# Kernel tuning notes

Measured on AMD Instinct MI355X. Metric: run time of the kernel, lower is better.

## Reference

```python
import jax, jax.numpy as jnp
import numpy as np

B, L, D, OUT, EXP = 4, 4096, 128, 55, 2
D2 = 2 * D

def _ln(x, g, b):
    m = jnp.mean(x, axis=-1, keepdims=True)
    v = jnp.mean((x - m) ** 2, axis=-1, keepdims=True)
    return (x - m) / jnp.sqrt(v + 1e-5) * g + b

def setup_inputs() -> dict:
    key = jax.random.key(0)
    ks = iter(jax.random.split(key, 32))
    w = lambda shape: jax.random.normal(next(ks), shape, jnp.float32) * 0.02
    inp = {
        'x1': jax.random.normal(next(ks), (B, L, D), jnp.float32),
        'x2': jax.random.normal(next(ks), (B, L, D), jnp.float32),
        'ln1_g': jnp.ones((D,)), 'ln1_b': jnp.zeros((D,)),
        'ln2_g': jnp.ones((D,)), 'ln2_b': jnp.zeros((D,)),
        'Wq': w((D, D)), 'bq': jnp.zeros((D,)),
        'Wv1': w((D, D)), 'bv1': jnp.zeros((D,)),
        'Wk': w((D, D)), 'bk': jnp.zeros((D,)),
        'Wv2': w((D, D)), 'bv2': jnp.zeros((D,)),
        'Wp1': w((D, D)), 'bp1': jnp.zeros((D,)),
        'Wp2': w((D, D)), 'bp2': jnp.zeros((D,)),
        'lnf_g': jnp.ones((D2,)), 'lnf_b': jnp.zeros((D2,)),
        'Wf1': w((D2, EXP * D2)), 'bf1': jnp.zeros((EXP * D2,)),
        'Wf2': w((EXP * D2, D2)), 'bf2': jnp.zeros((D2,)),
        'ln3_g': jnp.ones((D2,)), 'ln3_b': jnp.zeros((D2,)),
        'Wo': w((D2, OUT)), 'bo': jnp.zeros((OUT,)),
    }
    return inp

def reference(x1, x2, ln1_g, ln1_b, ln2_g, ln2_b, Wq, bq, Wv1, bv1, Wk, bk,
              Wv2, bv2, Wp1, bp1, Wp2, bp2, lnf_g, lnf_b, Wf1, bf1, Wf2, bf2,
              ln3_g, ln3_b, Wo, bo):
    res1, res2 = x1, x2
    x1n = _ln(x1, ln1_g, ln1_b)
    x2n = _ln(x2, ln2_g, ln2_b)
    q1 = x1n @ Wq + bq        # [B,L,D]
    v1 = x1n @ Wv1 + bv1
    k2 = x2n @ Wk + bk
    v2 = x2n @ Wv2 + bv2
    # faithful to torch: energy = einsum('bqd,bkd->bqk', keys2, queries1)
    energy = jnp.einsum('bqd,bkd->bqk', k2, q1)
    att = jax.nn.softmax(energy / jnp.sqrt(jnp.float32(D)), axis=-1)  # [B,L,L]
    out1 = jnp.einsum('bal,blv->bav', att, v1) @ Wp1 + bp1
    out2 = jnp.einsum('bal,blv->bav', att, v2) @ Wp2 + bp2
    y1 = out1 + res1
    y2 = out2 + res2
    x = jnp.concatenate([y1, y2], axis=-1)  # [B,L,2D]
    res = x
    h = _ln(x, lnf_g, lnf_b)
    h = jax.nn.gelu(h @ Wf1 + bf1, approximate=False) @ Wf2 + bf2
    x = _ln(h + res, ln3_g, ln3_b)
    return x @ Wo + bo  # [B,L,OUT]
```

## Files before the change

kernel.cpp:

```cpp
#include <hip/hip_runtime.h>
#include <hip/hip_fp16.h>

typedef _Float16 half8 __attribute__((ext_vector_type(8)));
typedef _Float16 half4 __attribute__((ext_vector_type(4)));
typedef float f32x4 __attribute__((ext_vector_type(4)));
typedef float f32x16 __attribute__((ext_vector_type(16)));
typedef int  i32x8 __attribute__((ext_vector_type(8)));
typedef long lng2 __attribute__((ext_vector_type(2)));

#define B_   4
#define L_   4096
#define D_   128
#define M_   (B_*L_)
#define D2_  256
#define H_   512
#define OUT_ 55

__device__ __forceinline__ f32x4 mfma16(half8 a, half8 b, f32x4 c) {
    return __builtin_amdgcn_mfma_f32_16x16x32_f16(a, b, c, 0, 0, 0);
}
__device__ __forceinline__ f32x16 mfma_mx32(i32x8 a, i32x8 b, f32x16 c) {
    return __builtin_amdgcn_mfma_scale_f32_32x32x64_f8f6f4(a, b, c, 0, 0, 0, 127, 0, 127);
}
__device__ __forceinline__ int pk4(float a, float b, float c, float d) {
    int t = __builtin_amdgcn_cvt_pk_fp8_f32(a, b, 0, false);
    return __builtin_amdgcn_cvt_pk_fp8_f32(c, d, t, true);
}
__device__ __forceinline__ float fexp2(float x) { return __builtin_amdgcn_exp2f(x); }

#define KSCL (0.08838834764831845f * 1.4426950408889634f)

#define WQ_OFF   0
#define WV1_OFF  16384
#define WK_OFF   32768
#define WV2_OFF  49152
#define WP1_OFF  65536
#define WP2_OFF  81920
#define WF1_OFF  98304
#define WF2_OFF  229376
#define WO_OFF   360448


__global__ void prep_kernel(const float* Wq, const float* Wv1, const float* Wk,
                            const float* Wv2, const float* Wp1, const float* Wp2,
                            const float* Wf1, const float* Wf2, const float* Wo,
                            _Float16* wsw, float* rowsum) {
    int id = blockIdx.y;
    int t  = blockIdx.x * 256 + threadIdx.x;
    if (id == 9) {
        if (t < 4096) ((f32x4*)rowsum)[t] = f32x4{0.f, 0.f, 0.f, 0.f};
        return;
    }
    const float* src = nullptr; int K = 0, N = 0, Npad = 0, off = 0;
    switch (id) {
        case 0: src = Wq;  K = 128; N = 128; Npad = 128; off = WQ_OFF;  break;
        case 1: src = Wv1; K = 128; N = 128; Npad = 128; off = WV1_OFF; break;
        case 2: src = Wk;  K = 128; N = 128; Npad = 128; off = WK_OFF;  break;
        case 3: src = Wv2; K = 128; N = 128; Npad = 128; off = WV2_OFF; break;
        case 4: src = Wp1; K = 128; N = 128; Npad = 128; off = WP1_OFF; break;
        case 5: src = Wp2; K = 128; N = 128; Npad = 128; off = WP2_OFF; break;
        case 6: src = Wf1; K = 256; N = 512; Npad = 512; off = WF1_OFF; break;
        case 7: src = Wf2; K = 512; N = 256; Npad = 256; off = WF2_OFF; break;
        case 8: src = Wo;  K = 256; N = 55;  Npad = 64;  off = WO_OFF;  break;
        default: return;
    }
    int total = K * Npad;
    if (t >= total) return;
    int k = t / Npad, n = t % Npad;
    float v = (n < N) ? src[k * N + n] : 0.f;
    int s = k >> 5, c = n >> 4, ln = n & 15;
    int q, j;
    if (id == 4 || id == 5) { q = (k >> 2) & 3; j = (k & 3) + (((k >> 4) & 1) << 2); }
    else                    { q = (k >> 3) & 3; j = k & 7; }
    int nc = Npad >> 4;
    wsw[off + ((size_t)((s * nc + c) * 64 + q * 16 + ln)) * 8 + j] = (_Float16)v;
}


__global__ __launch_bounds__(256) void proj_kernel(const float* x1, const float* x2,
        const _Float16* wsw,
        const float* ln1_g, const float* ln1_b, const float* ln2_g, const float* ln2_b,
        const float* bq, const float* bv1, const float* bk, const float* bv2,
        _Float16* q1, _Float16* k2, unsigned char* vsw8) {
    int g2 = blockIdx.y;
    const float* X  = g2 ? x2 : x1;
    const float* lg = g2 ? ln2_g : ln1_g;
    const float* lb = g2 ? ln2_b : ln1_b;
    int wave = threadIdx.x >> 6, lane = threadIdx.x & 63;
    int quad = lane >> 4, ln = lane & 15;
    int mbase = blockIdx.x * 64 + wave * 16;
    int lt = mbase >> 4;

    const float* xr = X + (size_t)(mbase + ln) * D_;
    float xv[4][8];
    float sum = 0.f, sq = 0.f;
    #pragma unroll
    for (int s = 0; s < 4; s++) {
        f32x4 v0 = *(const f32x4*)(xr + s * 32 + quad * 8);
        f32x4 v1 = *(const f32x4*)(xr + s * 32 + quad * 8 + 4);
        #pragma unroll
        for (int j = 0; j < 4; j++) {
            xv[s][j]     = v0[j];
            xv[s][j + 4] = v1[j];
            sum += v0[j] + v1[j];
            sq  += v0[j] * v0[j] + v1[j] * v1[j];
        }
    }
    sum += __shfl_xor(sum, 16); sum += __shfl_xor(sum, 32);
    sq  += __shfl_xor(sq, 16);  sq  += __shfl_xor(sq, 32);
    float mean = sum * (1.f / 128.f);
    float var  = sq * (1.f / 128.f) - mean * mean;
    float inv  = rsqrtf(var + 1e-5f);
    half8 a[4];
    #pragma unroll
    for (int s = 0; s < 4; s++) {
        f32x4 g0 = *(const f32x4*)(lg + s * 32 + quad * 8);
        f32x4 g1 = *(const f32x4*)(lg + s * 32 + quad * 8 + 4);
        f32x4 b0 = *(const f32x4*)(lb + s * 32 + quad * 8);
        f32x4 b1 = *(const f32x4*)(lb + s * 32 + quad * 8 + 4);
        #pragma unroll
        for (int j = 0; j < 4; j++) {
            a[s][j]     = (_Float16)((xv[s][j] - mean) * inv * g0[j] + b0[j]);
            a[s][j + 4] = (_Float16)((xv[s][j + 4] - mean) * inv * g1[j] + b1[j]);
        }
    }

    {
        const _Float16* Bw = wsw + (g2 ? WK_OFF : WQ_OFF);
        const float* bias = g2 ? bk : bq;
        float scl = g2 ? KSCL : 1.f;
        _Float16* out = g2 ? k2 : q1;
        f32x4 acc[8];
        #pragma unroll
        for (int c = 0; c < 8; c++) acc[c] = f32x4{0.f, 0.f, 0.f, 0.f};
        half8 Wc[4], Wn[4];
        #pragma unroll
        for (int s = 0; s < 4; s++)
            Wc[s] = *(const half8*)(Bw + ((size_t)((s * 8 + 0) * 64 + lane)) * 8);
        #pragma unroll
        for (int c = 0; c < 8; c++) {
            int cn = (c < 7) ? c + 1 : 7;
            #pragma unroll
            for (int s = 0; s < 4; s++)
                Wn[s] = *(const half8*)(Bw + ((size_t)((s * 8 + cn) * 64 + lane)) * 8);
            #pragma unroll
            for (int s = 0; s < 4; s++)
                acc[c] = mfma16(a[s], Wc[s], acc[c]);
            #pragma unroll
            for (int s = 0; s < 4; s++) Wc[s] = Wn[s];
        }
        #pragma unroll
        for (int c = 0; c < 8; c++) {
            int n = c * 16 + ln;
            float bv = bias[n];
            #pragma unroll
            for (int r = 0; r < 4; r++) {
                int s_o = c >> 1, q_o = ((c & 1) << 1) | (ln >> 3), j = ln & 7;
                out[((size_t)((lt * 4 + s_o) * 64 + q_o * 16 + (quad * 4 + r))) * 8 + j]
                    = (_Float16)((acc[c][r] + bv) * scl);
            }
        }
    }

    {
        const _Float16* Bw = wsw + (g2 ? WV2_OFF : WV1_OFF);
        const float* bias = g2 ? bv2 : bv1;
        int cbase = g2 ? 8 : 0;
        f32x4 acc[8];
        #pragma unroll
        for (int c = 0; c < 8; c++) acc[c] = f32x4{0.f, 0.f, 0.f, 0.f};
        half8 Wc[4], Wn[4];
        #pragma unroll
        for (int s = 0; s < 4; s++)
            Wc[s] = *(const half8*)(Bw + ((size_t)((s * 8 + 0) * 64 + lane)) * 8);
        #pragma unroll
        for (int c = 0; c < 8; c++) {
            int cn = (c < 7) ? c + 1 : 7;
            #pragma unroll
            for (int s = 0; s < 4; s++)
                Wn[s] = *(const half8*)(Bw + ((size_t)((s * 8 + cn) * 64 + lane)) * 8);
            #pragma unroll
            for (int s = 0; s < 4; s++)
                acc[c] = mfma16(a[s], Wc[s], acc[c]);
            #pragma unroll
            for (int s = 0; s < 4; s++) Wc[s] = Wn[s];
        }
        int b = mbase >> 12;
        int k64 = (mbase & (L_ - 1)) >> 6;
        int gg = quad >> 1, jh = quad & 1;
        unsigned char* Vb = vsw8 + (size_t)b * (1u << 20);
        #pragma unroll
        for (int c = 0; c < 8; c++) {
            int n = c * 16 + ln;
            float bv = bias[n];
            int pk = pk4(acc[c][0] + bv, acc[c][1] + bv, acc[c][2] + bv, acc[c][3] + bv);
            int v32 = (cbase + c) >> 1;
            int lane32 = ((c & 1) << 4) + ln + 32 * gg;
            *(int*)(Vb + ((size_t)((k64 * 8 + v32) * 64 + lane32)) * 32 + 16 * jh + 4 * wave) = pk;
        }
    }
}

__global__ __launch_bounds__(256) void score_kernel(
        const _Float16* __restrict__ q1sw, const _Float16* __restrict__ k2sw,
        unsigned char* __restrict__ pmat8, float* __restrict__ rowsum) {
    int w = threadIdx.x >> 6, lane = threadIdx.x & 63;
    int quad = lane >> 4, ln = lane & 15;
    int b = blockIdx.z;
    int id0 = blockIdx.y * 32 + blockIdx.x;
    int id  = ((id0 & 7) << 7) + (id0 >> 3);
    int bx = id & 31, by = id >> 5;
    int kL0 = by * 128 + (w & 1) * 64;
    int mL0 = bx * 128 + (w >> 1) * 64;
    int ltk = ((b << 12) + kL0) >> 4;
    int ltm = ((b << 12) + mL0) >> 4;

    f32x4 acc[4][4];
    #pragma unroll
    for (int i = 0; i < 4; i++)
        #pragma unroll
        for (int j = 0; j < 4; j++) acc[i][j] = f32x4{0.f, 0.f, 0.f, 0.f};

    #pragma unroll
    for (int s = 0; s < 4; s++) {
        half8 a[4], bq[4];
        #pragma unroll
        for (int i = 0; i < 4; i++)
            a[i] = *(const half8*)(q1sw + ((size_t)(((ltk + i) * 4 + s) * 64 + lane)) * 8);
        #pragma unroll
        for (int j = 0; j < 4; j++)
            bq[j] = *(const half8*)(k2sw + ((size_t)(((ltm + j) * 4 + s) * 64 + lane)) * 8);
        #pragma unroll
        for (int i = 0; i < 4; i++)
            #pragma unroll
            for (int j = 0; j < 4; j++)
                acc[i][j] = mfma16(a[i], bq[j], acc[i][j]);
    }

    unsigned char* Pb = pmat8 + (size_t)b * (16u << 20);
    int k64 = kL0 >> 6;
    int gg = quad >> 1, jh = quad & 1;
    #pragma unroll
    for (int j = 0; j < 4; j++) {
        int4 d;
        float csum = 0.f;
        #pragma unroll
        for (int i = 0; i < 4; i++) {
            float p0 = fexp2(acc[i][j][0]);
            float p1 = fexp2(acc[i][j][1]);
            float p2 = fexp2(acc[i][j][2]);
            float p3 = fexp2(acc[i][j][3]);
            csum += (p0 + p1) + (p2 + p3);
            ((int*)&d)[i] = pk4(p0, p1, p2, p3);
        }
        csum += __shfl_xor(csum, 16);
        csum += __shfl_xor(csum, 32);
        if (lane < 16)
            atomicAdd(&rowsum[(b << 12) + mL0 + j * 16 + ln], csum);
        int att32 = (mL0 >> 5) + (j >> 1);
        int a32 = ((j & 1) << 4) + ln;
        *(int4*)(Pb + ((size_t)((att32 * 64 + k64) * 64 + a32 + 32 * gg)) * 32 + 16 * jh) = d;
    }
}

__global__ __launch_bounds__(512) void pv_kernel(
        const unsigned char* __restrict__ pmat8, const unsigned char* __restrict__ vsw8,
        const float* __restrict__ rowsum,
        _Float16* __restrict__ att1, _Float16* __restrict__ att2) {
    __shared__ f32x4 part[4][2][4][64];
    int w = threadIdx.x >> 6, lane = threadIdx.x & 63;
    int wc = w & 3, kh = w >> 2;
    int id0 = blockIdx.x;
    int bid = ((id0 & 7) << 6) + (id0 >> 3);
    int rowG0 = bid * 32;
    int b = rowG0 >> 12;
    int att32 = (rowG0 & (L_ - 1)) >> 5;
    const unsigned char* Pb = pmat8 + (size_t)b * (16u << 20);
    const unsigned char* Vb = vsw8 + (size_t)b * (1u << 20);

    const unsigned char* Vbase = Vb + (size_t)(wc * 2) * 2048 + (size_t)lane * 32;
    const unsigned char* Pbase = Pb + (size_t)att32 * 131072 + (size_t)lane * 32;
    int sp0 = kh * 32;

    f32x16 acc0, acc1;
    #pragma unroll
    for (int i = 0; i < 16; i++) { acc0[i] = 0.f; acc1[i] = 0.f; }

    #define PVLOAD(dA, dB, dP, sp) do {                                       \
        dA = *(const i32x8*)(Vbase + (size_t)(sp) * 16384);                   \
        dB = *(const i32x8*)(Vbase + (size_t)(sp) * 16384 + 2048);            \
        dP = *(const i32x8*)(Pbase + (size_t)(sp) * 2048);                    \
    } while (0)

    i32x8 a0, b0, p0, a1, b1, p1, na, nb, np;
    PVLOAD(a0, b0, p0, sp0);
    PVLOAD(a1, b1, p1, sp0 + 1);
    for (int ii = 0; ii < 32; ii += 2) {
        int s2 = sp0 + ((ii + 2 < 32) ? ii + 2 : 30);
        int s3 = sp0 + ((ii + 3 < 32) ? ii + 3 : 31);
        PVLOAD(na, nb, np, s2);
        __builtin_amdgcn_s_setprio(1);
        acc0 = mfma_mx32(a0, p0, acc0);
        acc1 = mfma_mx32(b0, p0, acc1);
        __builtin_amdgcn_s_setprio(0);
        a0 = na; b0 = nb; p0 = np;
        PVLOAD(na, nb, np, s3);
        __builtin_amdgcn_s_setprio(1);
        acc0 = mfma_mx32(a1, p1, acc0);
        acc1 = mfma_mx32(b1, p1, acc1);
        __builtin_amdgcn_s_setprio(0);
        a1 = na; b1 = nb; p1 = np;
    }
    #undef PVLOAD

    if (kh == 1) {
        #pragma unroll
        for (int q = 0; q < 4; q++) {
            part[wc][0][q][lane] = f32x4{acc0[q * 4 + 0], acc0[q * 4 + 1],
                                         acc0[q * 4 + 2], acc0[q * 4 + 3]};
            part[wc][1][q][lane] = f32x4{acc1[q * 4 + 0], acc1[q * 4 + 1],
                                         acc1[q * 4 + 2], acc1[q * 4 + 3]};
        }
    }
    __syncthreads();
    if (kh == 0) {
        int aglob = rowG0 + (lane & 31);
        float inv = 1.f / rowsum[aglob];
        int g = lane >> 5;
        int lt = aglob >> 4, lnr = lane & 15;
        #pragma unroll
        for (int t = 0; t < 2; t++) {
            int v32 = wc * 2 + t;
            _Float16* att = (v32 >= 4) ? att2 : att1;
            int s = v32 & 3;
            #pragma unroll
            for (int q = 0; q < 4; q++) {
                f32x4 pp = part[wc][t][q][lane];
                half4 hv;
                #pragma unroll
                for (int rr = 0; rr < 4; rr++) {
                    float v = ((t == 0) ? acc0[q * 4 + rr] : acc1[q * 4 + rr]) + pp[rr];
                    hv[rr] = (_Float16)(v * inv);
                }
                *(half4*)(att + ((size_t)((lt * 4 + s) * 64 + q * 16 + lnr)) * 8 + 4 * g) = hv;
            }
        }
    }
}

__global__ __launch_bounds__(256) void attn_out_kernel(const _Float16* att1, const _Float16* att2,
        const _Float16* wsw, const float* bp1, const float* bp2,
        const float* x1, const float* x2, const float* lnf_g, const float* lnf_b,
        _Float16* res, _Float16* xn) {
    __shared__ float sst[2][16][2][2];
    int w = threadIdx.x >> 6, lane = threadIdx.x & 63;
    int quad = lane >> 4, ln = lane & 15;
    int rt = w & 1, st = w >> 1;
    int mbase = blockIdx.x * 32 + rt * 16;
    int lt = mbase >> 4;
    const _Float16* att = st ? att2 : att1;
    const _Float16* Wp = wsw + (st ? WP2_OFF : WP1_OFF);
    const float* bp = st ? bp2 : bp1;
    const float* xres = st ? x2 : x1;

    half8 a[4];
    #pragma unroll
    for (int s = 0; s < 4; s++)
        a[s] = *(const half8*)(att + ((size_t)((lt * 4 + s) * 64 + lane)) * 8);

    f32x4 y[8];
    #pragma unroll
    for (int c = 0; c < 8; c++) y[c] = f32x4{0,0,0,0};

    half8 Wc[4], Wn[4];
    #pragma unroll
    for (int s = 0; s < 4; s++)
        Wc[s] = *(const half8*)(Wp + ((size_t)((s * 8 + 0) * 64 + lane)) * 8);
    #pragma unroll
    for (int c = 0; c < 8; c++) {
        int cn = (c < 7) ? c + 1 : 7;
        #pragma unroll
        for (int s = 0; s < 4; s++)
            Wn[s] = *(const half8*)(Wp + ((size_t)((s * 8 + cn) * 64 + lane)) * 8);
        #pragma unroll
        for (int s = 0; s < 4; s++)
            y[c] = mfma16(a[s], Wc[s], y[c]);
        #pragma unroll
        for (int s = 0; s < 4; s++) Wc[s] = Wn[s];
    }

    float psum[4] = {0,0,0,0}, psq[4] = {0,0,0,0};
    #pragma unroll
    for (int c = 0; c < 8; c++) {
        int n = c * 16 + ln;
        float bv = bp[n];
        #pragma unroll
        for (int r = 0; r < 4; r++) {
            int m = mbase + quad * 4 + r;
            float v = y[c][r] + bv + xres[(size_t)m * D_ + n];
            y[c][r] = v; psum[r] += v; psq[r] += v * v;
        }
    }
    #pragma unroll
    for (int off = 1; off < 16; off <<= 1)
        #pragma unroll
        for (int r = 0; r < 4; r++) { psum[r] += __shfl_xor(psum[r], off); psq[r] += __shfl_xor(psq[r], off); }
    if (ln == 0)
        #pragma unroll
        for (int r = 0; r < 4; r++) {
            sst[rt][quad * 4 + r][st][0] = psum[r];
            sst[rt][quad * 4 + r][st][1] = psq[r];
        }
    __syncthreads();
    #pragma unroll
    for (int r = 0; r < 4; r++) {
        float su = sst[rt][quad * 4 + r][0][0] + sst[rt][quad * 4 + r][1][0];
        float sq = sst[rt][quad * 4 + r][0][1] + sst[rt][quad * 4 + r][1][1];
        float mean = su * (1.f / 256.f);
        float var = sq * (1.f / 256.f) - mean * mean;
        float inv = rsqrtf(var + 1e-5f);
        int m = mbase + quad * 4 + r;
        int lt_m = m >> 4;
        #pragma unroll
        for (int c = 0; c < 8; c++) {
            int colg = st * 128 + c * 16 + ln;
            res[(size_t)m * D2_ + colg] = (_Float16)y[c][r];
            float yn = (y[c][r] - mean) * inv * lnf_g[colg] + lnf_b[colg];
            int s_x = colg >> 5, q_x = (colg >> 3) & 3, j = colg & 7;
            xn[((size_t)((lt_m * 8 + s_x) * 64 + q_x * 16 + (m & 15))) * 8 + j] = (_Float16)yn;
        }
    }
}

__global__ __launch_bounds__(256) void ffn1_kernel(const _Float16* xn, const _Float16* wsw,
        const float* bf1, _Float16* h) {
    int wave = threadIdx.x >> 6, lane = threadIdx.x & 63;
    int quad = lane >> 4, ln = lane & 15;
    int mbase = blockIdx.x * 64 + wave * 16;
    int lt = mbase >> 4;
    int nt = blockIdx.y;
    const _Float16* W = wsw + WF1_OFF;

    half8 a[8];
    #pragma unroll
    for (int s = 0; s < 8; s++)
        a[s] = *(const half8*)(xn + ((size_t)((lt * 8 + s) * 64 + lane)) * 8);

    f32x4 acc[8];
    #pragma unroll
    for (int c = 0; c < 8; c++) acc[c] = f32x4{0,0,0,0};

    half8 Wc[8], Wn[8];
    #pragma unroll
    for (int s = 0; s < 8; s++)
        Wc[s] = *(const half8*)(W + ((size_t)((s * 32 + nt * 8) * 64 + lane)) * 8);
    #pragma unroll
    for (int c = 0; c < 8; c++) {
        int cn = (c < 7) ? c + 1 : 7;
        #pragma unroll
        for (int s = 0; s < 8; s++)
            Wn[s] = *(const half8*)(W + ((size_t)((s * 32 + nt * 8 + cn) * 64 + lane)) * 8);
        #pragma unroll
        for (int s = 0; s < 8; s++)
            acc[c] = mfma16(a[s], Wc[s], acc[c]);
        #pragma unroll
        for (int s = 0; s < 8; s++) Wc[s] = Wn[s];
    }
    #pragma unroll
    for (int c = 0; c < 8; c++) {
        int n = nt * 128 + c * 16 + ln;
        float bv = bf1[n];
        int s_h = n >> 5, q_h = (n >> 3) & 3, j = n & 7;
        #pragma unroll
        for (int r = 0; r < 4; r++) {
            float v = acc[c][r] + bv;
            float u = 0.7978845608f * (v + 0.044715f * v * v * v);
            float e = fexp2(-2.8853900818f * u);
            float ge = v * __builtin_amdgcn_rcpf(1.f + e);
            h[((size_t)((lt * 16 + s_h) * 64 + q_h * 16 + (quad * 4 + r))) * 8 + j] = (_Float16)ge;
        }
    }
}

__global__ __launch_bounds__(256) void ffn2_out_kernel(const _Float16* h, const _Float16* wsw,
        const float* bf2, const _Float16* res, const float* g3, const float* b3,
        const float* bo, float* out) {
    __shared__ float sst[2][16][2][2];
    __shared__ _Float16 xt[8192];
    __shared__ f32x4 pc[2][4][64];
    int w = threadIdx.x >> 6, lane = threadIdx.x & 63;
    int quad = lane >> 4, ln = lane & 15;
    int rt = w & 1, nh = w >> 1;
    int mb = blockIdx.x * 32 + rt * 16;
    int lt = mb >> 4;
    const _Float16* W = wsw + WF2_OFF;

    f32x4 acc[8];
    #pragma unroll
    for (int c = 0; c < 8; c++) acc[c] = f32x4{0,0,0,0};

    half8 aC, aN;
    half8 Wc[8], Wn[8];
    aC = *(const half8*)(h + ((size_t)((lt * 16 + 0) * 64 + lane)) * 8);
    #pragma unroll
    for (int c = 0; c < 8; c++)
        Wc[c] = *(const half8*)(W + ((size_t)((0 * 16 + nh * 8 + c) * 64 + lane)) * 8);

    #pragma unroll
    for (int s = 0; s < 16; s++) {
        int sn = (s < 15) ? s + 1 : 15;
        aN = *(const half8*)(h + ((size_t)((lt * 16 + sn) * 64 + lane)) * 8);
        #pragma unroll
        for (int c = 0; c < 8; c++)
            Wn[c] = *(const half8*)(W + ((size_t)((sn * 16 + nh * 8 + c) * 64 + lane)) * 8);
        #pragma unroll
        for (int c = 0; c < 8; c++)
            acc[c] = mfma16(aC, Wc[c], acc[c]);
        aC = aN;
        #pragma unroll
        for (int c = 0; c < 8; c++) Wc[c] = Wn[c];
    }

    float y[8][4];
    float psum[4] = {0,0,0,0}, psq[4] = {0,0,0,0};
    #pragma unroll
    for (int c = 0; c < 8; c++) {
        int n = nh * 128 + c * 16 + ln;
        float bv = bf2[n];
        #pragma unroll
        for (int r = 0; r < 4; r++) {
            int m = mb + quad * 4 + r;
            float v = acc[c][r] + bv + (float)res[(size_t)m * D2_ + n];
            y[c][r] = v; psum[r] += v; psq[r] += v * v;
        }
    }
    #pragma unroll
    for (int off = 1; off < 16; off <<= 1)
        #pragma unroll
        for (int r = 0; r < 4; r++) { psum[r] += __shfl_xor(psum[r], off); psq[r] += __shfl_xor(psq[r], off); }
    if (ln == 0)
        #pragma unroll
        for (int r = 0; r < 4; r++) { sst[rt][quad * 4 + r][nh][0] = psum[r]; sst[rt][quad * 4 + r][nh][1] = psq[r]; }
    __syncthreads();
    #pragma unroll
    for (int r = 0; r < 4; r++) {
        float su = sst[rt][quad * 4 + r][0][0] + sst[rt][quad * 4 + r][1][0];
        float sq = sst[rt][quad * 4 + r][0][1] + sst[rt][quad * 4 + r][1][1];
        float mean = su * (1.f / 256.f);
        float var = sq * (1.f / 256.f) - mean * mean;
        float invs = rsqrtf(var + 1e-5f);
        #pragma unroll
        for (int c = 0; c < 8; c++) {
            int n = nh * 128 + c * 16 + ln;
            float yn = (y[c][r] - mean) * invs * g3[n] + b3[n];
            int s_x = n >> 5, q_x = (n >> 3) & 3, j = n & 7;
            xt[((rt * 8 + s_x) * 64 + q_x * 16 + (quad * 4 + r)) * 8 + j] = (_Float16)yn;
        }
    }
    __syncthreads();

    int rt2 = w & 1, kh = w >> 1;
    const _Float16* Wo = wsw + WO_OFF;
    f32x4 oacc[4];
    #pragma unroll
    for (int c = 0; c < 4; c++) oacc[c] = f32x4{0,0,0,0};
    #pragma unroll
    for (int ss = 0; ss < 4; ss++) {
        int s = kh * 4 + ss;
        half8 a = *(const half8*)(xt + ((size_t)((rt2 * 8 + s) * 64 + lane)) * 8);
        #pragma unroll
        for (int c = 0; c < 4; c++)
            oacc[c] = mfma16(a, *(const half8*)(Wo + ((size_t)((s * 4 + c) * 64 + lane)) * 8), oacc[c]);
    }
    if (kh == 1)
        #pragma unroll
        for (int c = 0; c < 4; c++) pc[rt2][c][lane] = oacc[c];
    __syncthreads();
    if (kh == 0) {
        int mb2 = blockIdx.x * 32 + rt2 * 16;
        #pragma unroll
        for (int c = 0; c < 4; c++) {
            f32x4 p = pc[rt2][c][lane];
            int n = c * 16 + ln;
            if (n < OUT_) {
                float bv = bo[n];
                #pragma unroll
                for (int r = 0; r < 4; r++)
                    out[(size_t)(mb2 + quad * 4 + r) * OUT_ + n] = oacc[c][r] + p[r] + bv;
            }
        }
    }
}

extern "C" void kernel_launch(void* const* d_in, const int* in_sizes, int n_in,
                              void* d_out, int out_size, void* d_ws, size_t ws_size,
                              hipStream_t stream) {
    const float* x1    = (const float*)d_in[0];
    const float* x2    = (const float*)d_in[1];
    const float* ln1_g = (const float*)d_in[2];
    const float* ln1_b = (const float*)d_in[3];
    const float* ln2_g = (const float*)d_in[4];
    const float* ln2_b = (const float*)d_in[5];
    const float* Wq    = (const float*)d_in[6];
    const float* bq    = (const float*)d_in[7];
    const float* Wv1   = (const float*)d_in[8];
    const float* bv1   = (const float*)d_in[9];
    const float* Wk    = (const float*)d_in[10];
    const float* bk    = (const float*)d_in[11];
    const float* Wv2   = (const float*)d_in[12];
    const float* bv2   = (const float*)d_in[13];
    const float* Wp1   = (const float*)d_in[14];
    const float* bp1   = (const float*)d_in[15];
    const float* Wp2   = (const float*)d_in[16];
    const float* bp2   = (const float*)d_in[17];
    const float* lnf_g = (const float*)d_in[18];
    const float* lnf_b = (const float*)d_in[19];
    const float* Wf1   = (const float*)d_in[20];
    const float* bf1   = (const float*)d_in[21];
    const float* Wf2   = (const float*)d_in[22];
    const float* bf2   = (const float*)d_in[23];
    const float* ln3_g = (const float*)d_in[24];
    const float* ln3_b = (const float*)d_in[25];
    const float* Wo    = (const float*)d_in[26];
    const float* bo    = (const float*)d_in[27];
    float* out = (float*)d_out;

    char* ws = (char*)d_ws;
    const size_t MB = 1 << 20;
    _Float16* q1sw   = (_Float16*)(ws + 0 * MB);
    _Float16* k2sw   = (_Float16*)(ws + 4 * MB);
    unsigned char* vsw8 = (unsigned char*)(ws + 8 * MB);
    _Float16* att1   = (_Float16*)(ws + 12 * MB);
    _Float16* att2   = (_Float16*)(ws + 16 * MB);
    _Float16* wsw    = (_Float16*)(ws + 28 * MB);
    float*    rowsum = (float*)   (ws + 29 * MB);
    _Float16* res    = (_Float16*)(ws + 30 * MB);
    _Float16* xn     = (_Float16*)(ws + 46 * MB);
    _Float16* h      = (_Float16*)(ws + 54 * MB);
    unsigned char* pmat8 = (unsigned char*)(ws + 78 * MB);

    prep_kernel<<<dim3(512, 10), 256, 0, stream>>>(Wq, Wv1, Wk, Wv2, Wp1, Wp2, Wf1, Wf2, Wo,
                                                   wsw, rowsum);
    proj_kernel<<<dim3(M_ / 64, 2), 256, 0, stream>>>(x1, x2, wsw,
                                                      ln1_g, ln1_b, ln2_g, ln2_b,
                                                      bq, bv1, bk, bv2,
                                                      q1sw, k2sw, vsw8);
    score_kernel<<<dim3(32, 32, 4), 256, 0, stream>>>(q1sw, k2sw, pmat8, rowsum);
    pv_kernel<<<dim3(M_ / 32), 512, 0, stream>>>(pmat8, vsw8, rowsum, att1, att2);
    attn_out_kernel<<<dim3(M_ / 32), 256, 0, stream>>>(att1, att2, wsw, bp1, bp2,
                                                       x1, x2, lnf_g, lnf_b, res, xn);
    ffn1_kernel<<<dim3(M_ / 64, 4), 256, 0, stream>>>(xn, wsw, bf1, h);
    ffn2_out_kernel<<<dim3(M_ / 32), 256, 0, stream>>>(h, wsw, bf2, res, ln3_g, ln3_b, bo, out);
}
```

Baseline: 233.5 us.

## Fuse FFN1 and FFN2+output kernels, keeping hidden activations in shared memory

Merges the two FFN kernels into one 512-thread block per 32 rows. The GELU hidden activations are written to a 32KB shared-memory tile instead of a global buffer, so the 16K×512 fp16 round trip and one launch go away. The work is re-split so 8 waves share the FFN2 N-dimension and the output projection K-dimension, which needs an extra partial-sum reduction. In exchange, the explicit register double-buffering of weight loads is dropped, and the larger shared-memory footprint and block size may lower occupancy.

After: 228.4 us. 2.2% less time.

```diff
diff --git a/kernel.cpp b/kernel.cpp
--- a/kernel.cpp
+++ b/kernel.cpp
@@ -432,161 +432,139 @@
     }
 }
 
-__global__ __launch_bounds__(256) void ffn1_kernel(const _Float16* xn, const _Float16* wsw,
-        const float* bf1, _Float16* h) {
-    int wave = threadIdx.x >> 6, lane = threadIdx.x & 63;
-    int quad = lane >> 4, ln = lane & 15;
-    int mbase = blockIdx.x * 64 + wave * 16;
-    int lt = mbase >> 4;
-    int nt = blockIdx.y;
-    const _Float16* W = wsw + WF1_OFF;
-
-    half8 a[8];
-    #pragma unroll
-    for (int s = 0; s < 8; s++)
-        a[s] = *(const half8*)(xn + ((size_t)((lt * 8 + s) * 64 + lane)) * 8);
-
-    f32x4 acc[8];
-    #pragma unroll
-    for (int c = 0; c < 8; c++) acc[c] = f32x4{0,0,0,0};
-
-    half8 Wc[8], Wn[8];
-    #pragma unroll
-    for (int s = 0; s < 8; s++)
-        Wc[s] = *(const half8*)(W + ((size_t)((s * 32 + nt * 8) * 64 + lane)) * 8);
-    #pragma unroll
-    for (int c = 0; c < 8; c++) {
-        int cn = (c < 7) ? c + 1 : 7;
-        #pragma unroll
-        for (int s = 0; s < 8; s++)
-            Wn[s] = *(const half8*)(W + ((size_t)((s * 32 + nt * 8 + cn) * 64 + lane)) * 8);
-        #pragma unroll
-        for (int s = 0; s < 8; s++)
-            acc[c] = mfma16(a[s], Wc[s], acc[c]);
-        #pragma unroll
-        for (int s = 0; s < 8; s++) Wc[s] = Wn[s];
-    }
-    #pragma unroll
-    for (int c = 0; c < 8; c++) {
-        int n = nt * 128 + c * 16 + ln;
-        float bv = bf1[n];
-        int s_h = n >> 5, q_h = (n >> 3) & 3, j = n & 7;
-        #pragma unroll
-        for (int r = 0; r < 4; r++) {
-            float v = acc[c][r] + bv;
-            float u = 0.7978845608f * (v + 0.044715f * v * v * v);
-            float e = fexp2(-2.8853900818f * u);
-            float ge = v * __builtin_amdgcn_rcpf(1.f + e);
-            h[((size_t)((lt * 16 + s_h) * 64 + q_h * 16 + (quad * 4 + r))) * 8 + j] = (_Float16)ge;
-        }
-    }
-}
-
-__global__ __launch_bounds__(256) void ffn2_out_kernel(const _Float16* h, const _Float16* wsw,
-        const float* bf2, const _Float16* res, const float* g3, const float* b3,
-        const float* bo, float* out) {
-    __shared__ float sst[2][16][2][2];
+__global__ __launch_bounds__(512) void ffn_kernel(const _Float16* xn, const _Float16* wsw,
+        const float* bf1, const float* bf2, const _Float16* res,
+        const float* g3, const float* b3, const float* bo, float* out) {
+    __shared__ _Float16 hT[16384];
+    __shared__ float sst[2][16][4][2];
     __shared__ _Float16 xt[8192];
-    __shared__ f32x4 pc[2][4][64];
+    __shared__ f32x4 pc[2][3][4][64];
     int w = threadIdx.x >> 6, lane = threadIdx.x & 63;
     int quad = lane >> 4, ln = lane & 15;
     int rt = w & 1, nh = w >> 1;
-    int mb = blockIdx.x * 32 + rt * 16;
-    int lt = mb >> 4;
-    const _Float16* W = wsw + WF2_OFF;
-
-    f32x4 acc[8];
-    #pragma unroll
-    for (int c = 0; c < 8; c++) acc[c] = f32x4{0,0,0,0};
-
-    half8 aC, aN;
-    half8 Wc[8], Wn[8];
-    aC = *(const half8*)(h + ((size_t)((lt * 16 + 0) * 64 + lane)) * 8);
-    #pragma unroll
-    for (int c = 0; c < 8; c++)
-        Wc[c] = *(const half8*)(W + ((size_t)((0 * 16 + nh * 8 + c) * 64 + lane)) * 8);
-
-    #pragma unroll
-    for (int s = 0; s < 16; s++) {
-        int sn = (s < 15) ? s + 1 : 15;
-        aN = *(const half8*)(h + ((size_t)((lt * 16 + sn) * 64 + lane)) * 8);
-        #pragma unroll
-        for (int c = 0; c < 8; c++)
-            Wn[c] = *(const half8*)(W + ((size_t)((sn * 16 + nh * 8 + c) * 64 + lane)) * 8);
-        #pragma unroll
-        for (int c = 0; c < 8; c++)
-            acc[c] = mfma16(aC, Wc[c], acc[c]);
-        aC = aN;
-        #pragma unroll
-        for (int c = 0; c < 8; c++) Wc[c] = Wn[c];
-    }
-
-    float y[8][4];
-    float psum[4] = {0,0,0,0}, psq[4] = {0,0,0,0};
-    #pragma unroll
-    for (int c = 0; c < 8; c++) {
-        int n = nh * 128 + c * 16 + ln;
-        float bv = bf2[n];
-        #pragma unroll
-        for (int r = 0; r < 4; r++) {
-            int m = mb + quad * 4 + r;
-            float v = acc[c][r] + bv + (float)res[(size_t)m * D2_ + n];
-            y[c][r] = v; psum[r] += v; psq[r] += v * v;
-        }
-    }
-    #pragma unroll
-    for (int off = 1; off < 16; off <<= 1)
-        #pragma unroll
-        for (int r = 0; r < 4; r++) { psum[r] += __shfl_xor(psum[r], off); psq[r] += __shfl_xor(psq[r], off); }
-    if (ln == 0)
-        #pragma unroll
-        for (int r = 0; r < 4; r++) { sst[rt][quad * 4 + r][nh][0] = psum[r]; sst[rt][quad * 4 + r][nh][1] = psq[r]; }
+    int mb = blockIdx.x * 32;
+    int ltg = (mb + rt * 16) >> 4;
+
+    {
+        const _Float16* W = wsw + WF1_OFF;
+        half8 a[8];
+        #pragma unroll
+        for (int s = 0; s < 8; s++)
+            a[s] = *(const half8*)(xn + ((size_t)((ltg * 8 + s) * 64 + lane)) * 8);
+        f32x4 acc[8];
+        #pragma unroll
+        for (int c = 0; c < 8; c++) acc[c] = f32x4{0,0,0,0};
+        #pragma unroll
+        for (int c = 0; c < 8; c++) {
+            #pragma unroll
+            for (int s = 0; s < 8; s++) {
+                half8 Wf = *(const half8*)(W + ((size_t)((s * 32 + nh * 8 + c) * 64 + lane)) * 8);
+                acc[c] = mfma16(a[s], Wf, acc[c]);
+            }
+        }
+        #pragma unroll
+        for (int c = 0; c < 8; c++) {
+            int n = nh * 128 + c * 16 + ln;
+            float bv = bf1[n];
+            int s_h = n >> 5, q_h = (n >> 3) & 3, j = n & 7;
+            #pragma unroll
+            for (int r = 0; r < 4; r++) {
+                float v = acc[c][r] + bv;
+                float u = 0.7978845608f * (v + 0.044715f * v * v * v);
+                float e = fexp2(-2.8853900818f * u);
+                float ge = v * __builtin_amdgcn_rcpf(1.f + e);
+                hT[((rt * 16 + s_h) * 64 + q_h * 16 + (quad * 4 + r)) * 8 + j] = (_Float16)ge;
+            }
+        }
+    }
     __syncthreads();
+
+    float y[4][4];
+    {
+        const _Float16* W = wsw + WF2_OFF;
+        f32x4 acc[4];
+        #pragma unroll
+        for (int c = 0; c < 4; c++) acc[c] = f32x4{0,0,0,0};
+        #pragma unroll
+        for (int s = 0; s < 16; s++) {
+            half8 a = *(const half8*)(hT + ((size_t)((rt * 16 + s) * 64 + lane)) * 8);
+            #pragma unroll
+            for (int c = 0; c < 4; c++) {
+                half8 Wf = *(const half8*)(W + ((size_t)((s * 16 + nh * 4 + c) * 64 + lane)) * 8);
+                acc[c] = mfma16(a, Wf, acc[c]);
+            }
+        }
+        float psum[4] = {0,0,0,0}, psq[4] = {0,0,0,0};
+        #pragma unroll
+        for (int c = 0; c < 4; c++) {
+            int n = nh * 64 + c * 16 + ln;
+            float bv = bf2[n];
+            #pragma unroll
+            for (int r = 0; r < 4; r++) {
+                int m = mb + rt * 16 + quad * 4 + r;
+                float v = acc[c][r] + bv + (float)res[(size_t)m * D2_ + n];
+                y[c][r] = v; psum[r] += v; psq[r] += v * v;
+            }
+        }
+        #pragma unroll
+        for (int off = 1; off < 16; off <<= 1)
+            #pragma unroll
+            for (int r = 0; r < 4; r++) { psum[r] += __shfl_xor(psum[r], off); psq[r] += __shfl_xor(psq[r], off); }
+        if (ln == 0)
+            #pragma unroll
+            for (int r = 0; r < 4; r++) { sst[rt][quad * 4 + r][nh][0] = psum[r]; sst[rt][quad * 4 + r][nh][1] = psq[r]; }
+    }
+    __syncthreads();
     #pragma unroll
     for (int r = 0; r < 4; r++) {
-        float su = sst[rt][quad * 4 + r][0][0] + sst[rt][quad * 4 + r][1][0];
-        float sq = sst[rt][quad * 4 + r][0][1] + sst[rt][quad * 4 + r][1][1];
+        int row = quad * 4 + r;
+        float su = sst[rt][row][0][0] + sst[rt][row][1][0] + sst[rt][row][2][0] + sst[rt][row][3][0];
+        float sq = sst[rt][row][0][1] + sst[rt][row][1][1] + sst[rt][row][2][1] + sst[rt][row][3][1];
         float mean = su * (1.f / 256.f);
         float var = sq * (1.f / 256.f) - mean * mean;
         float invs = rsqrtf(var + 1e-5f);
         #pragma unroll
-        for (int c = 0; c < 8; c++) {
-            int n = nh * 128 + c * 16 + ln;
+        for (int c = 0; c < 4; c++) {
+            int n = nh * 64 + c * 16 + ln;
             float yn = (y[c][r] - mean) * invs * g3[n] + b3[n];
             int s_x = n >> 5, q_x = (n >> 3) & 3, j = n & 7;
-            xt[((rt * 8 + s_x) * 64 + q_x * 16 + (quad * 4 + r)) * 8 + j] = (_Float16)yn;
+            xt[((rt * 8 + s_x) * 64 + q_x * 16 + row) * 8 + j] = (_Float16)yn;
         }
     }
     __syncthreads();
 
-    int rt2 = w & 1, kh = w >> 1;
-    const _Float16* Wo = wsw + WO_OFF;
-    f32x4 oacc[4];
-    #pragma unroll
-    for (int c = 0; c < 4; c++) oacc[c] = f32x4{0,0,0,0};
-    #pragma unroll
-    for (int ss = 0; ss < 4; ss++) {
-        int s = kh * 4 + ss;
-        half8 a = *(const half8*)(xt + ((size_t)((rt2 * 8 + s) * 64 + lane)) * 8);
-        #pragma unroll
-        for (int c = 0; c < 4; c++)
-            oacc[c] = mfma16(a, *(const half8*)(Wo + ((size_t)((s * 4 + c) * 64 + lane)) * 8), oacc[c]);
-    }
-    if (kh == 1)
-        #pragma unroll
-        for (int c = 0; c < 4; c++) pc[rt2][c][lane] = oacc[c];
-    __syncthreads();
-    if (kh == 0) {
-        int mb2 = blockIdx.x * 32 + rt2 * 16;
-        #pragma unroll
-        for (int c = 0; c < 4; c++) {
-            f32x4 p = pc[rt2][c][lane];
-            int n = c * 16 + ln;
-            if (n < OUT_) {
-                float bv = bo[n];
-                #pragma unroll
-                for (int r = 0; r < 4; r++)
-                    out[(size_t)(mb2 + quad * 4 + r) * OUT_ + n] = oacc[c][r] + p[r] + bv;
+    {
+        int kh = nh;
+        const _Float16* Wo = wsw + WO_OFF;
+        f32x4 oacc[4];
+        #pragma unroll
+        for (int c = 0; c < 4; c++) oacc[c] = f32x4{0,0,0,0};
+        #pragma unroll
+        for (int ss = 0; ss < 2; ss++) {
+            int s = kh * 2 + ss;
+            half8 a = *(const half8*)(xt + ((size_t)((rt * 8 + s) * 64 + lane)) * 8);
+            #pragma unroll
+            for (int c = 0; c < 4; c++)
+                oacc[c] = mfma16(a, *(const half8*)(Wo + ((size_t)((s * 4 + c) * 64 + lane)) * 8), oacc[c]);
+        }
+        if (kh > 0)
+            #pragma unroll
+            for (int c = 0; c < 4; c++) pc[rt][kh - 1][c][lane] = oacc[c];
+        __syncthreads();
+        if (kh == 0) {
+            #pragma unroll
+            for (int c = 0; c < 4; c++) {
+                f32x4 p0 = pc[rt][0][c][lane];
+                f32x4 p1 = pc[rt][1][c][lane];
+                f32x4 p2 = pc[rt][2][c][lane];
+                int n = c * 16 + ln;
+                if (n < OUT_) {
+                    float bv = bo[n];
+                    #pragma unroll
+                    for (int r = 0; r < 4; r++)
+                        out[(size_t)(mb + rt * 16 + quad * 4 + r) * OUT_ + n]
+                            = oacc[c][r] + p0[r] + p1[r] + p2[r] + bv;
+                }
             }
         }
     }
@@ -636,7 +614,6 @@
     float*    rowsum = (float*)   (ws + 29 * MB);
     _Float16* res    = (_Float16*)(ws + 30 * MB);
     _Float16* xn     = (_Float16*)(ws + 46 * MB);
-    _Float16* h      = (_Float16*)(ws + 54 * MB);
     unsigned char* pmat8 = (unsigned char*)(ws + 78 * MB);
 
     prep_kernel<<<dim3(512, 10), 256, 0, stream>>>(Wq, Wv1, Wk, Wv2, Wp1, Wp2, Wf1, Wf2, Wo,
@@ -649,6 +626,6 @@
     pv_kernel<<<dim3(M_ / 32), 512, 0, stream>>>(pmat8, vsw8, rowsum, att1, att2);
     attn_out_kernel<<<dim3(M_ / 32), 256, 0, stream>>>(att1, att2, wsw, bp1, bp2,
                                                        x1, x2, lnf_g, lnf_b, res, xn);
-    ffn1_kernel<<<dim3(M_ / 64, 4), 256, 0, stream>>>(xn, wsw, bf1, h);
-    ffn2_out_kernel<<<dim3(M_ / 32), 256, 0, stream>>>(h, wsw, bf2, res, ln3_g, ln3_b, bo, out);
-}
+    ffn_kernel<<<dim3(M_ / 32), 512, 0, stream>>>(xn, wsw, bf1, bf2, res,
+                                                  ln3_g, ln3_b, bo, out);
+}
```
